# Optimization experiments

Hardware: AMD Instinct MI355X
Metric: run time of the kernel (lower is better)

Reference implementation:

```python
import math
import jax, jax.numpy as jnp
import numpy as np

VOCAB = 50257
MAX_SEQ = 64
D_MODEL = 1024
N_HEADS = 16
N_LAYERS = 12
BATCH = 256
SEQ = 64


def setup_inputs() -> dict:
    key = jax.random.key(0)
    ks = jax.random.split(key, 16)
    s = 0.02
    d, L = D_MODEL, N_LAYERS
    inp = {
        "idx": jax.random.randint(ks[0], (BATCH, SEQ), 0, VOCAB, dtype=jnp.int32),
        "tok_emb": jax.random.normal(ks[1], (VOCAB, d), jnp.float32) * s,
        "pos_emb": jax.random.normal(ks[2], (MAX_SEQ, d), jnp.float32) * s,
        # per-block params stacked over layer dim [L, ...]; linear as x @ W + b
        "wqkv": jax.random.normal(ks[3], (L, d, 3 * d), jnp.float32) * s,
        "bqkv": jnp.zeros((L, 3 * d), jnp.float32),
        "wo": jax.random.normal(ks[4], (L, d, d), jnp.float32) * s,
        "bo": jnp.zeros((L, d), jnp.float32),
        "w1": jax.random.normal(ks[5], (L, d, 4 * d), jnp.float32) * s,
        "b1": jnp.zeros((L, 4 * d), jnp.float32),
        "w2": jax.random.normal(ks[6], (L, 4 * d, d), jnp.float32) * s,
        "b2": jnp.zeros((L, d), jnp.float32),
        "ln_g": jnp.ones((d,), jnp.float32),
        "ln_b": jnp.zeros((d,), jnp.float32),
        "out_w": jax.random.normal(ks[7], (d, d), jnp.float32) * s,
        "out_b": jnp.zeros((d,), jnp.float32),
    }
    return inp


def _attention(x, wqkv_l, bqkv_l, wo_l, bo_l):
    B, S, d = x.shape
    H = N_HEADS
    dh = d // H
    qkv = x @ wqkv_l + bqkv_l                      # [B,S,3d]
    q, k, v = jnp.split(qkv, 3, axis=-1)
    q = q.reshape(B, S, H, dh).transpose(0, 2, 1, 3)  # [B,H,S,dh]
    k = k.reshape(B, S, H, dh).transpose(0, 2, 1, 3)
    v = v.reshape(B, S, H, dh).transpose(0, 2, 1, 3)
    # NOTE: original scales by sqrt(d_model), not sqrt(head_dim)
    attn = jnp.einsum("bhqd,bhkd->bhqk", q, k) / math.sqrt(d)
    causal = jnp.tril(jnp.ones((S, S), bool))       # query i attends key j<=i
    attn = jnp.where(causal[None, None], attn, -jnp.inf)
    # NOTE: original applies softmax over dim=-2 (the QUERY axis)
    attn = jax.nn.softmax(attn, axis=-2)
    y = jnp.einsum("bhqk,bhkd->bhqd", attn, v)      # [B,H,S,dh]
    y = y.transpose(0, 2, 1, 3).reshape(B, S, d)
    return y @ wo_l + bo_l


def _layer_norm(x, g, b, eps=1e-5):
    mu = jnp.mean(x, axis=-1, keepdims=True)
    var = jnp.var(x, axis=-1, keepdims=True)
    return (x - mu) * jax.lax.rsqrt(var + eps) * g + b


def reference(idx, tok_emb, pos_emb, wqkv, bqkv, wo, bo, w1, b1, w2, b2,
              ln_g, ln_b, out_w, out_b):
    S = idx.shape[1]
    x = tok_emb[idx] + pos_emb[:S]                 # [B,S,d]
    for l in range(N_LAYERS):
        x = _attention(x, wqkv[l], bqkv[l], wo[l], bo[l]) + x
        h = jax.nn.gelu(x @ w1[l] + b1[l], approximate=False)
        x = h @ w2[l] + b2[l] + x
    x = _layer_norm(x, ln_g, ln_b)
    return x @ out_w + out_b
```

## Files before the change

kernel.cpp:

```cpp
#include <hip/hip_runtime.h>
#include <stdint.h>

typedef unsigned short u16;
typedef __bf16 bf16x8 __attribute__((ext_vector_type(8)));
typedef float f32x4 __attribute__((ext_vector_type(4)));

#define MT 16384

__device__ __forceinline__ u16 f2bf(float f) {
  union { float f; unsigned u; } x; x.f = f;
  unsigned r = x.u + 0x7fffu + ((x.u >> 16) & 1u);
  return (u16)(r >> 16);
}

#pragma clang diagnostic push
#pragma clang diagnostic ignored "-Waddress-space-conversion"
typedef __attribute__((address_space(1))) unsigned as1u;
typedef __attribute__((address_space(3))) unsigned as3u;
__device__ __forceinline__ void stage16(const u16* g, u16* lbase) {
  __builtin_amdgcn_global_load_lds((as1u*)g, (as3u*)lbase, 16, 0, 0);
}
#pragma clang diagnostic pop

__global__ void __launch_bounds__(256)
transpose_cvt(const float* __restrict__ in, u16* __restrict__ out, int K, int N) {
  __shared__ float tile[32][33];
  const int k0 = blockIdx.y * 32, n0 = blockIdx.x * 32;
  const int tx = threadIdx.x, ty = threadIdx.y;
  #pragma unroll
  for (int r = 0; r < 32; r += 8)
    tile[ty + r][tx] = in[(size_t)(k0 + ty + r) * N + n0 + tx];
  __syncthreads();
  #pragma unroll
  for (int r = 0; r < 32; r += 8)
    out[(size_t)(n0 + ty + r) * K + k0 + tx] = f2bf(tile[tx][ty + r]);
}

__global__ void __launch_bounds__(256)
embed_kernel(const int* __restrict__ idx, const float* __restrict__ tok,
             const float* __restrict__ pos, float* __restrict__ x,
             u16* __restrict__ xb) {
  const int tk = blockIdx.x;
  const int s = tk & 63;
  const int id = idx[tk];
  const int t = threadIdx.x;
  float4 a = ((const float4*)(tok + (size_t)id * 1024))[t];
  float4 p = ((const float4*)(pos + (size_t)s * 1024))[t];
  float4 r; r.x = a.x + p.x; r.y = a.y + p.y; r.z = a.z + p.z; r.w = a.w + p.w;
  ((float4*)(x + (size_t)tk * 1024))[t] = r;
  u16* o = xb + (size_t)tk * 1024 + t * 4;
  o[0] = f2bf(r.x); o[1] = f2bf(r.y); o[2] = f2bf(r.z); o[3] = f2bf(r.w);
}

template<int EPI>
__global__ void __launch_bounds__(256, 3)
gemm128x256(const u16* __restrict__ A, const u16* __restrict__ Bt,
            const float* __restrict__ bias, float* __restrict__ resf,
            u16* __restrict__ outb, float* __restrict__ outf,
            int M, int N, int K, int gn) {
  __shared__ __align__(16) u16 lA[2][4096];
  __shared__ __align__(16) u16 lB[2][8192];
  const int t = threadIdx.x;
  const int lane = t & 63, w = t >> 6;
  const int fr = lane & 15, fg = lane >> 4;

  const int nwg = gridDim.x;
  const int bid = blockIdx.x;
  const int s = (bid & 7) * (nwg >> 3) + (bid >> 3);
  const int tn = s % gn, tm = s / gn;
  const int m0 = tm * 128, n0 = tn * 256;

  const int rin = ((lane >> 3) << 1) + ((lane >> 2) & 1);
  const int fgl = (lane & 3) ^ ((lane >> 3) & 3);
  const u16* gA[2]; const u16* gB[4];
  #pragma unroll
  for (int i = 0; i < 2; ++i)
    gA[i] = A + (size_t)(m0 + (w * 2 + i) * 16 + rin) * K + fgl * 8;
  #pragma unroll
  for (int j = 0; j < 4; ++j)
    gB[j] = Bt + (size_t)(n0 + (w * 4 + j) * 16 + rin) * K + fgl * 8;

  const int sub8 = ((fr & 1) * 4 + (fg ^ ((fr >> 1) & 3))) * 8;
  const int ar = (fr >> 1) * 64 + sub8;
  const int br = (w * 32 + (fr >> 1)) * 64 + sub8;

  f32x4 acc[8][4] = {};
  const int NT = K >> 5;

  #pragma unroll
  for (int i = 0; i < 2; ++i) stage16(gA[i], &lA[0][(w * 2 + i) * 512]);
  #pragma unroll
  for (int j = 0; j < 4; ++j) stage16(gB[j], &lB[0][(w * 4 + j) * 512]);
  __syncthreads();

  int cur = 0;
  for (int kt = 0; kt < NT; ++kt) {
    if (kt + 1 < NT) {
      const int ko = (kt + 1) << 5;
      #pragma unroll
      for (int i = 0; i < 2; ++i) stage16(gA[i] + ko, &lA[cur ^ 1][(w * 2 + i) * 512]);
      #pragma unroll
      for (int j = 0; j < 4; ++j) stage16(gB[j] + ko, &lB[cur ^ 1][(w * 4 + j) * 512]);
    }
    bf16x8 af[8], bv[4];
    #pragma unroll
    for (int m = 0; m < 8; ++m) af[m] = *(const bf16x8*)&lA[cur][m * 512 + ar];
    #pragma unroll
    for (int n = 0; n < 4; ++n) bv[n] = *(const bf16x8*)&lB[cur][n * 512 + br];
    #pragma unroll
    for (int m = 0; m < 8; ++m)
      #pragma unroll
      for (int n = 0; n < 4; ++n)
        acc[m][n] = __builtin_amdgcn_mfma_f32_16x16x32_bf16(af[m], bv[n], acc[m][n], 0, 0, 0);
    __syncthreads();
    cur ^= 1;
  }

  #pragma unroll
  for (int m = 0; m < 8; ++m) {
    const int row = m0 + m * 16 + fg * 4;
    #pragma unroll
    for (int n = 0; n < 4; ++n) {
      const int col = n0 + w * 64 + n * 16 + fr;
      const float bc = bias[col];
      #pragma unroll
      for (int i = 0; i < 4; ++i) {
        const size_t off = (size_t)(row + i) * N + col;
        float v = acc[m][n][i] + bc;
        if constexpr (EPI == 0) {
          outb[off] = f2bf(v);
        } else if constexpr (EPI == 1) {
          v = 0.5f * v * (1.0f + erff(v * 0.70710678118654752f));
          outb[off] = f2bf(v);
        } else if constexpr (EPI == 2) {
          v += resf[off];
          resf[off] = v;
          outb[off] = f2bf(v);
        } else {
          outf[off] = v;
        }
      }
    }
  }
}

__global__ void __launch_bounds__(256)
attn_kernel(const u16* __restrict__ qkv, u16* __restrict__ y) {
  __shared__ __align__(16) u16 qs[64][72];
  __shared__ __align__(16) u16 ks[64][72];
  __shared__ __align__(16) u16 vts[64][72];
  __shared__ __align__(16) float S[64][68];
  __shared__ float red[4][64];

  const int h = blockIdx.x, b = blockIdx.y;
  const int t = threadIdx.x;
  const int lane = t & 63, w = t >> 6;
  const int fr = lane & 15, fg = lane >> 4;

  #pragma unroll
  for (int it = 0; it < 2; ++it) {
    const int id = t + it * 256;
    const int row = id >> 3, seg = id & 7;
    const size_t gq = (size_t)(b * 64 + row) * 3072 + h * 64 + seg * 8;
    *(uint4*)&qs[row][seg * 8] = *(const uint4*)&qkv[gq];
    *(uint4*)&ks[row][seg * 8] = *(const uint4*)&qkv[gq + 1024];
  }
  {
    const int d = t & 63;
    #pragma unroll
    for (int it = 0; it < 16; ++it) {
      const int s = (t >> 6) + it * 4;
      vts[d][s] = qkv[(size_t)(b * 64 + s) * 3072 + 2048 + h * 64 + d];
    }
  }
  __syncthreads();

  f32x4 sa[4] = {};
  #pragma unroll
  for (int kk = 0; kk < 64; kk += 32) {
    bf16x8 qa = *(const bf16x8*)&qs[w * 16 + fr][kk + fg * 8];
    #pragma unroll
    for (int n = 0; n < 4; ++n) {
      bf16x8 kb = *(const bf16x8*)&ks[n * 16 + fr][kk + fg * 8];
      sa[n] = __builtin_amdgcn_mfma_f32_16x16x32_bf16(qa, kb, sa[n], 0, 0, 0);
    }
  }
  #pragma unroll
  for (int n = 0; n < 4; ++n)
    #pragma unroll
    for (int i = 0; i < 4; ++i) {
      const int row = w * 16 + fg * 4 + i, col = n * 16 + fr;
      S[row][col] = (row >= col) ? sa[n][i] * 0.03125f : -1e30f;
    }
  __syncthreads();

  const int c = t & 63, q4 = t >> 6;
  float mx = -1e30f;
  float e[16];
  #pragma unroll
  for (int i = 0; i < 16; ++i) mx = fmaxf(mx, S[q4 * 16 + i][c]);
  red[q4][c] = mx;
  __syncthreads();
  mx = fmaxf(fmaxf(red[0][c], red[1][c]), fmaxf(red[2][c], red[3][c]));
  float sum = 0.f;
  #pragma unroll
  for (int i = 0; i < 16; ++i) { e[i] = __expf(S[q4 * 16 + i][c] - mx); sum += e[i]; }
  __syncthreads();
  red[q4][c] = sum;
  __syncthreads();
  sum = red[0][c] + red[1][c] + red[2][c] + red[3][c];
  const float inv = 1.0f / sum;
  u16 (*P)[72] = qs;
  #pragma unroll
  for (int i = 0; i < 16; ++i)
    P[q4 * 16 + i][c] = f2bf(e[i] * inv);
  __syncthreads();

  f32x4 oa[4] = {};
  #pragma unroll
  for (int kk = 0; kk < 64; kk += 32) {
    bf16x8 pa = *(const bf16x8*)&P[w * 16 + fr][kk + fg * 8];
    #pragma unroll
    for (int n = 0; n < 4; ++n) {
      bf16x8 vb = *(const bf16x8*)&vts[n * 16 + fr][kk + fg * 8];
      oa[n] = __builtin_amdgcn_mfma_f32_16x16x32_bf16(pa, vb, oa[n], 0, 0, 0);
    }
  }
  #pragma unroll
  for (int n = 0; n < 4; ++n)
    #pragma unroll
    for (int i = 0; i < 4; ++i) {
      const int row = w * 16 + fg * 4 + i, col = n * 16 + fr;
      y[(size_t)(b * 64 + row) * 1024 + h * 64 + col] = f2bf(oa[n][i]);
    }
}

__global__ void __launch_bounds__(256)
ln_kernel(const float* __restrict__ x, const float* __restrict__ g,
          const float* __restrict__ bb, u16* __restrict__ xn) {
  __shared__ float sred[8];
  const int tok = blockIdx.x;
  const int t = threadIdx.x;
  const float4 v = ((const float4*)(x + (size_t)tok * 1024))[t];
  float s  = v.x + v.y + v.z + v.w;
  float ss = v.x * v.x + v.y * v.y + v.z * v.z + v.w * v.w;
  #pragma unroll
  for (int o = 32; o > 0; o >>= 1) {
    s  += __shfl_xor(s, o);
    ss += __shfl_xor(ss, o);
  }
  const int w = t >> 6;
  if ((t & 63) == 0) { sred[w] = s; sred[4 + w] = ss; }
  __syncthreads();
  s  = sred[0] + sred[1] + sred[2] + sred[3];
  ss = sred[4] + sred[5] + sred[6] + sred[7];
  const float mu = s * (1.0f / 1024.0f);
  const float var = ss * (1.0f / 1024.0f) - mu * mu;
  const float rs = rsqrtf(var + 1e-5f);
  const float4 gg = ((const float4*)g)[t];
  const float4 b4 = ((const float4*)bb)[t];
  u16* o = xn + (size_t)tok * 1024 + t * 4;
  o[0] = f2bf((v.x - mu) * rs * gg.x + b4.x);
  o[1] = f2bf((v.y - mu) * rs * gg.y + b4.y);
  o[2] = f2bf((v.z - mu) * rs * gg.z + b4.z);
  o[3] = f2bf((v.w - mu) * rs * gg.w + b4.w);
}

extern "C" void kernel_launch(void* const* d_in, const int* in_sizes, int n_in,
                              void* d_out, int out_size, void* d_ws, size_t ws_size,
                              hipStream_t stream) {
  const int*   idx     = (const int*)  d_in[0];
  const float* tok_emb = (const float*)d_in[1];
  const float* pos_emb = (const float*)d_in[2];
  const float* wqkv    = (const float*)d_in[3];
  const float* bqkv    = (const float*)d_in[4];
  const float* wo      = (const float*)d_in[5];
  const float* bo      = (const float*)d_in[6];
  const float* w1      = (const float*)d_in[7];
  const float* b1      = (const float*)d_in[8];
  const float* w2      = (const float*)d_in[9];
  const float* b2      = (const float*)d_in[10];
  const float* ln_g    = (const float*)d_in[11];
  const float* ln_b    = (const float*)d_in[12];
  const float* out_w   = (const float*)d_in[13];
  const float* out_b   = (const float*)d_in[14];

  char* p = (char*)d_ws;
  auto take = [&](size_t n) { char* r = p; p += (n + 255) & ~(size_t)255; return r; };
  u16*   wqkv_t = (u16*)  take((size_t)1024 * 3072 * 2);
  u16*   wo_t   = (u16*)  take((size_t)1024 * 1024 * 2);
  u16*   w1_t   = (u16*)  take((size_t)1024 * 4096 * 2);
  u16*   w2_t   = (u16*)  take((size_t)4096 * 1024 * 2);
  u16*   wout_t = (u16*)  take((size_t)1024 * 1024 * 2);
  float* xf     = (float*)take((size_t)MT * 1024 * 4);
  u16*   xb     = (u16*)  take((size_t)MT * 1024 * 2);
  u16*   yb     = (u16*)  take((size_t)MT * 1024 * 2);
  u16*   big    = (u16*)  take((size_t)MT * 4096 * 2);

  const dim3 tb(32, 8);
  embed_kernel<<<MT, 256, 0, stream>>>(idx, tok_emb, pos_emb, xf, xb);

  for (int l = 0; l < 12; ++l) {
    transpose_cvt<<<dim3(3072 / 32, 1024 / 32), tb, 0, stream>>>(
        wqkv + (size_t)l * 1024 * 3072, wqkv_t, 1024, 3072);
    transpose_cvt<<<dim3(1024 / 32, 1024 / 32), tb, 0, stream>>>(
        wo + (size_t)l * 1024 * 1024, wo_t, 1024, 1024);
    transpose_cvt<<<dim3(4096 / 32, 1024 / 32), tb, 0, stream>>>(
        w1 + (size_t)l * 1024 * 4096, w1_t, 1024, 4096);
    transpose_cvt<<<dim3(1024 / 32, 4096 / 32), tb, 0, stream>>>(
        w2 + (size_t)l * 4096 * 1024, w2_t, 4096, 1024);

    gemm128x256<0><<<(MT / 128) * (3072 / 256), 256, 0, stream>>>(
        xb, wqkv_t, bqkv + (size_t)l * 3072,
        nullptr, big, nullptr, MT, 3072, 1024, 3072 / 256);
    attn_kernel<<<dim3(16, 256), 256, 0, stream>>>(big, yb);
    gemm128x256<2><<<(MT / 128) * (1024 / 256), 256, 0, stream>>>(
        yb, wo_t, bo + (size_t)l * 1024,
        xf, xb, nullptr, MT, 1024, 1024, 1024 / 256);
    gemm128x256<1><<<(MT / 128) * (4096 / 256), 256, 0, stream>>>(
        xb, w1_t, b1 + (size_t)l * 4096,
        nullptr, big, nullptr, MT, 4096, 1024, 4096 / 256);
    gemm128x256<2><<<(MT / 128) * (1024 / 256), 256, 0, stream>>>(
        big, w2_t, b2 + (size_t)l * 1024,
        xf, xb, nullptr, MT, 1024, 4096, 1024 / 256);
  }

  transpose_cvt<<<dim3(1024 / 32, 1024 / 32), tb, 0, stream>>>(out_w, wout_t, 1024, 1024);
  ln_kernel<<<MT, 256, 0, stream>>>(xf, ln_g, ln_b, yb);
  gemm128x256<3><<<(MT / 128) * (1024 / 256), 256, 0, stream>>>(
      yb, wout_t, out_b, nullptr, nullptr, (float*)d_out, MT, 1024, 1024, 1024 / 256);
}
```

Before: 7.462 ms.

## Shrink GEMM tile to 128x128 with 2x2 wave layout

Replaces the 128x256 GEMM block tile with a 128x128 tile, arranging the four waves in a 2x2 grid of 64x64 subtiles. This halves the B shared-memory buffer and the per-thread accumulators, which should improve occupancy, and doubles the number of blocks. The cost is lower operand reuse per LDS read and more global loads of A across the extra N tiles.

New measurement: 7.221 ms. 3.2% less time.

```diff
diff --git a/kernel.cpp b/kernel.cpp
--- a/kernel.cpp
+++ b/kernel.cpp
@@ -17,7 +17,7 @@
 #pragma clang diagnostic ignored "-Waddress-space-conversion"
 typedef __attribute__((address_space(1))) unsigned as1u;
 typedef __attribute__((address_space(3))) unsigned as3u;
-__device__ __forceinline__ void stage16(const u16* g, u16* lbase) {
+__device__ __forceinline__ void stage16(const u16* g, const u16* lbase) {
   __builtin_amdgcn_global_load_lds((as1u*)g, (as3u*)lbase, 16, 0, 0);
 }
 #pragma clang diagnostic pop
@@ -54,43 +54,44 @@
 
 template<int EPI>
 __global__ void __launch_bounds__(256, 3)
-gemm128x256(const u16* __restrict__ A, const u16* __restrict__ Bt,
-            const float* __restrict__ bias, float* __restrict__ resf,
-            u16* __restrict__ outb, float* __restrict__ outf,
-            int M, int N, int K, int gn) {
+gemm128(const u16* __restrict__ A, const u16* __restrict__ Bt,
+        const float* __restrict__ bias, float* __restrict__ resf,
+        u16* __restrict__ outb, float* __restrict__ outf,
+        int M, int N, int K, int gn) {
   __shared__ __align__(16) u16 lA[2][4096];
-  __shared__ __align__(16) u16 lB[2][8192];
+  __shared__ __align__(16) u16 lB[2][4096];
   const int t = threadIdx.x;
   const int lane = t & 63, w = t >> 6;
+  const int wr = w >> 1, wc = w & 1;
   const int fr = lane & 15, fg = lane >> 4;
 
   const int nwg = gridDim.x;
   const int bid = blockIdx.x;
   const int s = (bid & 7) * (nwg >> 3) + (bid >> 3);
   const int tn = s % gn, tm = s / gn;
-  const int m0 = tm * 128, n0 = tn * 256;
+  const int m0 = tm * 128, n0 = tn * 128;
 
   const int rin = ((lane >> 3) << 1) + ((lane >> 2) & 1);
   const int fgl = (lane & 3) ^ ((lane >> 3) & 3);
-  const u16* gA[2]; const u16* gB[4];
-  #pragma unroll
-  for (int i = 0; i < 2; ++i)
-    gA[i] = A + (size_t)(m0 + (w * 2 + i) * 16 + rin) * K + fgl * 8;
-  #pragma unroll
-  for (int j = 0; j < 4; ++j)
-    gB[j] = Bt + (size_t)(n0 + (w * 4 + j) * 16 + rin) * K + fgl * 8;
+  const u16* gA[2]; const u16* gB[2];
+  #pragma unroll
+  for (int i = 0; i < 2; ++i) {
+    gA[i] = A  + (size_t)(m0 + (w * 2 + i) * 16 + rin) * K + fgl * 8;
+    gB[i] = Bt + (size_t)(n0 + (w * 2 + i) * 16 + rin) * K + fgl * 8;
+  }
 
   const int sub8 = ((fr & 1) * 4 + (fg ^ ((fr >> 1) & 3))) * 8;
-  const int ar = (fr >> 1) * 64 + sub8;
-  const int br = (w * 32 + (fr >> 1)) * 64 + sub8;
-
-  f32x4 acc[8][4] = {};
+  const int ar = wr * 2048 + (fr >> 1) * 64 + sub8;
+  const int br = wc * 2048 + (fr >> 1) * 64 + sub8;
+
+  f32x4 acc[4][4] = {};
   const int NT = K >> 5;
 
   #pragma unroll
-  for (int i = 0; i < 2; ++i) stage16(gA[i], &lA[0][(w * 2 + i) * 512]);
-  #pragma unroll
-  for (int j = 0; j < 4; ++j) stage16(gB[j], &lB[0][(w * 4 + j) * 512]);
+  for (int i = 0; i < 2; ++i) {
+    stage16(gA[i], &lA[0][(w * 2 + i) * 512]);
+    stage16(gB[i], &lB[0][(w * 2 + i) * 512]);
+  }
   __syncthreads();
 
   int cur = 0;
@@ -98,17 +99,18 @@
     if (kt + 1 < NT) {
       const int ko = (kt + 1) << 5;
       #pragma unroll
-      for (int i = 0; i < 2; ++i) stage16(gA[i] + ko, &lA[cur ^ 1][(w * 2 + i) * 512]);
-      #pragma unroll
-      for (int j = 0; j < 4; ++j) stage16(gB[j] + ko, &lB[cur ^ 1][(w * 4 + j) * 512]);
-    }
-    bf16x8 af[8], bv[4];
-    #pragma unroll
-    for (int m = 0; m < 8; ++m) af[m] = *(const bf16x8*)&lA[cur][m * 512 + ar];
-    #pragma unroll
-    for (int n = 0; n < 4; ++n) bv[n] = *(const bf16x8*)&lB[cur][n * 512 + br];
-    #pragma unroll
-    for (int m = 0; m < 8; ++m)
+      for (int i = 0; i < 2; ++i) {
+        stage16(gA[i] + ko, &lA[cur ^ 1][(w * 2 + i) * 512]);
+        stage16(gB[i] + ko, &lB[cur ^ 1][(w * 2 + i) * 512]);
+      }
+    }
+    bf16x8 af[4], bv[4];
+    #pragma unroll
+    for (int m = 0; m < 4; ++m) af[m] = *(const bf16x8*)&lA[cur][ar + m * 512];
+    #pragma unroll
+    for (int n = 0; n < 4; ++n) bv[n] = *(const bf16x8*)&lB[cur][br + n * 512];
+    #pragma unroll
+    for (int m = 0; m < 4; ++m)
       #pragma unroll
       for (int n = 0; n < 4; ++n)
         acc[m][n] = __builtin_amdgcn_mfma_f32_16x16x32_bf16(af[m], bv[n], acc[m][n], 0, 0, 0);
@@ -117,11 +119,11 @@
   }
 
   #pragma unroll
-  for (int m = 0; m < 8; ++m) {
-    const int row = m0 + m * 16 + fg * 4;
+  for (int m = 0; m < 4; ++m) {
+    const int row = m0 + wr * 64 + m * 16 + fg * 4;
     #pragma unroll
     for (int n = 0; n < 4; ++n) {
-      const int col = n0 + w * 64 + n * 16 + fr;
+      const int col = n0 + wc * 64 + n * 16 + fr;
       const float bc = bias[col];
       #pragma unroll
       for (int i = 0; i < 4; ++i) {
@@ -310,23 +312,23 @@
     transpose_cvt<<<dim3(1024 / 32, 4096 / 32), tb, 0, stream>>>(
         w2 + (size_t)l * 4096 * 1024, w2_t, 4096, 1024);
 
-    gemm128x256<0><<<(MT / 128) * (3072 / 256), 256, 0, stream>>>(
+    gemm128<0><<<(MT / 128) * (3072 / 128), 256, 0, stream>>>(
         xb, wqkv_t, bqkv + (size_t)l * 3072,
-        nullptr, big, nullptr, MT, 3072, 1024, 3072 / 256);
+        nullptr, big, nullptr, MT, 3072, 1024, 3072 / 128);
     attn_kernel<<<dim3(16, 256), 256, 0, stream>>>(big, yb);
-    gemm128x256<2><<<(MT / 128) * (1024 / 256), 256, 0, stream>>>(
+    gemm128<2><<<(MT / 128) * (1024 / 128), 256, 0, stream>>>(
         yb, wo_t, bo + (size_t)l * 1024,
-        xf, xb, nullptr, MT, 1024, 1024, 1024 / 256);
-    gemm128x256<1><<<(MT / 128) * (4096 / 256), 256, 0, stream>>>(
+        xf, xb, nullptr, MT, 1024, 1024, 1024 / 128);
+    gemm128<1><<<(MT / 128) * (4096 / 128), 256, 0, stream>>>(
         xb, w1_t, b1 + (size_t)l * 4096,
-        nullptr, big, nullptr, MT, 4096, 1024, 4096 / 256);
-    gemm128x256<2><<<(MT / 128) * (1024 / 256), 256, 0, stream>>>(
+        nullptr, big, nullptr, MT, 4096, 1024, 4096 / 128);
+    gemm128<2><<<(MT / 128) * (1024 / 128), 256, 0, stream>>>(
         big, w2_t, b2 + (size_t)l * 1024,
-        xf, xb, nullptr, MT, 1024, 4096, 1024 / 256);
+        xf, xb, nullptr, MT, 1024, 4096, 1024 / 128);
   }
 
   transpose_cvt<<<dim3(1024 / 32, 1024 / 32), tb, 0, stream>>>(out_w, wout_t, 1024, 1024);
   ln_kernel<<<MT, 256, 0, stream>>>(xf, ln_g, ln_b, yb);
-  gemm128x256<3><<<(MT / 128) * (1024 / 256), 256, 0, stream>>>(
-      yb, wout_t, out_b, nullptr, nullptr, (float*)d_out, MT, 1024, 1024, 1024 / 256);
-}
+  gemm128<3><<<(MT / 128) * (1024 / 128), 256, 0, stream>>>(
+      yb, wout_t, out_b, nullptr, nullptr, (float*)d_out, MT, 1024, 1024, 1024 / 128);
+}
```
